# Performance work log

Measured on AMD Instinct MI355X. Metric: run time of the kernel, lower is better.

Reference implementation:

```python
import jax, jax.numpy as jnp
import numpy as np
import math

D_MODEL = 1024
N_HEADS = 16
D_HEAD = D_MODEL // N_HEADS
B, S = 4, 2048


def setup_inputs() -> dict:
    key = jax.random.key(0)
    ks = jax.random.split(key, 9)
    std = 1.0 / math.sqrt(D_MODEL)
    x = jax.random.normal(ks[0], (B, S, D_MODEL), dtype=jnp.float32)
    # causal mask: True = masked out
    mask = jnp.triu(jnp.ones((S, S), dtype=bool), k=1)
    Wq = jax.random.normal(ks[1], (D_MODEL, D_MODEL), jnp.float32) * std
    bq = jnp.zeros((D_MODEL,), jnp.float32)
    Wk = jax.random.normal(ks[2], (D_MODEL, D_MODEL), jnp.float32) * std
    bk = jnp.zeros((D_MODEL,), jnp.float32)
    Wv = jax.random.normal(ks[3], (D_MODEL, D_MODEL), jnp.float32) * std
    bv = jnp.zeros((D_MODEL,), jnp.float32)
    Wo = jax.random.normal(ks[4], (D_MODEL, D_MODEL), jnp.float32) * std
    bo = jnp.zeros((D_MODEL,), jnp.float32)
    return {"x": x, "mask": mask, "Wq": Wq, "bq": bq, "Wk": Wk, "bk": bk,
            "Wv": Wv, "bv": bv, "Wo": Wo, "bo": bo}


def reference(x, mask, Wq, bq, Wk, bk, Wv, bv, Wo, bo):
    b, s, _ = x.shape
    scale = math.sqrt(D_HEAD)
    # projections (Linear: x @ W.T + b), reshape to [b, h, s, d]
    def proj(W, bias):
        y = jnp.einsum('bsd,ed->bse', x, W) + bias
        return y.reshape(b, s, N_HEADS, D_HEAD).transpose(0, 2, 1, 3)
    q = proj(Wq, bq)
    k = proj(Wk, bk)
    v = proj(Wv, bv)
    scores = jnp.einsum('bhqd,bhkd->bhqk', q, k) / scale  # [b,h,s,s]
    scores = jnp.where(mask[None, None, :, :], -jnp.inf, scores)
    attn = jax.nn.softmax(scores, axis=-1)
    # dropout is identity in eval mode
    out = jnp.einsum('bhqk,bhkd->bhqd', attn, v)
    out = out.transpose(0, 2, 1, 3).reshape(b, s, D_MODEL)
    return jnp.einsum('bsd,ed->bse', out, Wo) + bo
```

## Files before the change

### kernel.cpp

```cpp
#include <hip/hip_runtime.h>
#include <stdint.h>

#define NH 16
#define DH 64
#define DM 1024
#define Bz 4
#define Sz 2048
#define NKT 16

typedef __bf16 bf16x8 __attribute__((ext_vector_type(8)));
typedef float f32x4 __attribute__((ext_vector_type(4)));
typedef float f32x16 __attribute__((ext_vector_type(16)));

#define GLD_LDS16(gsrc, ldst)                                             \
    __builtin_amdgcn_global_load_lds(                                     \
        (const __attribute__((address_space(1))) void*)(gsrc),            \
        (__attribute__((address_space(3))) void*)(ldst), 16, 0, 0)

__device__ __forceinline__ unsigned short f2bf(float f) {
    unsigned u = __float_as_uint(f);
    u += 0x7FFFu + ((u >> 16) & 1u);
    return (unsigned short)(u >> 16);
}
__device__ __forceinline__ float bf2f(unsigned short h) {
    return __uint_as_float(((unsigned)h) << 16);
}
__device__ __forceinline__ unsigned pack2bf(float a, float b) {
    return (unsigned)f2bf(a) | ((unsigned)f2bf(b) << 16);
}

__global__ void detect_dtype(const unsigned short* __restrict__ xs,
                             int* __restrict__ flagp)
{
    const int t = threadIdx.x;
    int cnt = 0;
    for (int i = 0; i < 64; i++) {
        const unsigned short h = xs[(t * 64 + i) * 2];
        const int e = (h >> 7) & 0xFF;
        if (h != 0 && e >= 100 && e <= 130) cnt++;
    }
#pragma unroll
    for (int off = 32; off >= 1; off >>= 1)
        cnt += __shfl_xor(cnt, off);
    if (t == 0) *flagp = (cnt < 2048) ? 1 : 0;
}

__global__ __launch_bounds__(256) void convert_inputs(
    const void* s0, const void* s1, const void* s2, const void* s3,
    const void* s4, const void* s5, const void* s6, const void* s7,
    const void* s8,
    unsigned short* d0, unsigned short* d1, unsigned short* d2,
    unsigned short* d3, unsigned short* d4, unsigned short* d5,
    unsigned short* d6, unsigned short* d7, unsigned short* d8,
    const int* __restrict__ flagp)
{
    const void* s; unsigned short* d; int n;
    switch (blockIdx.y) {
        case 0: s = s0; d = d0; n = Bz * Sz * DM; break;
        case 1: s = s1; d = d1; n = DM * DM; break;
        case 2: s = s2; d = d2; n = DM * DM; break;
        case 3: s = s3; d = d3; n = DM * DM; break;
        case 4: s = s4; d = d4; n = DM * DM; break;
        case 5: s = s5; d = d5; n = DM; break;
        case 6: s = s6; d = d6; n = DM; break;
        case 7: s = s7; d = d7; n = DM; break;
        default: s = s8; d = d8; n = DM; break;
    }
    const int flag   = *flagp;
    const int stride = gridDim.x * blockDim.x * 8;
    const int base   = (blockIdx.x * blockDim.x + threadIdx.x) * 8;
    if (flag) {
        const float* sf = (const float*)s;
        for (int i = base; i < n; i += stride) {
            const float4 v0 = *reinterpret_cast<const float4*>(&sf[i]);
            const float4 v1 = *reinterpret_cast<const float4*>(&sf[i + 4]);
            uint4 o;
            o.x = pack2bf(v0.x, v0.y);
            o.y = pack2bf(v0.z, v0.w);
            o.z = pack2bf(v1.x, v1.y);
            o.w = pack2bf(v1.z, v1.w);
            *reinterpret_cast<uint4*>(&d[i]) = o;
        }
    } else {
        const unsigned short* sh = (const unsigned short*)s;
        for (int i = base; i < n; i += stride)
            *reinterpret_cast<uint4*>(&d[i]) = *reinterpret_cast<const uint4*>(&sh[i]);
    }
}


__global__ __launch_bounds__(256, 2) void gemm_qkv(
    const unsigned short* __restrict__ X,
    const unsigned short* __restrict__ Wq,
    const unsigned short* __restrict__ Wk,
    const unsigned short* __restrict__ Wv,
    const unsigned short* __restrict__ bq,
    const unsigned short* __restrict__ bk,
    const unsigned short* __restrict__ bv,
    unsigned short* __restrict__ Qb,
    unsigned short* __restrict__ Kb,
    unsigned short* __restrict__ Vtb)
{
    __shared__ __align__(16) unsigned short As[2][128 * 64];
    __shared__ __align__(16) unsigned short Bs[2][128 * 64];

    const int tid  = threadIdx.x;
    const int w    = tid >> 6, lane = tid & 63;
    const int l31  = lane & 31, half = lane >> 5;
    const int wm   = (w & 1) * 64, wn = (w >> 1) * 64;

    const int flat = (int)(blockIdx.y * gridDim.x + blockIdx.x);
    const int k8   = flat & 7;
    const int m    = flat >> 3;
    const int proj = m >> 6;
    const int mm   = m & 63;
    const int bm   = (k8 * 8 + (mm >> 3)) * 128;
    const int bn   = (mm & 7) * 128;

    const unsigned short* W      = proj == 0 ? Wq : (proj == 1 ? Wk : Wv);
    const unsigned short* bias_p = proj == 0 ? bq : (proj == 1 ? bk : bv);
    const unsigned short* Abase  = X + (size_t)bm * DM;
    const unsigned short* Bbase  = W + (size_t)bn * DM;

    const int sr8 = lane >> 3;
    const int sce = ((lane & 7) ^ sr8) * 8;

    f32x16 acc[2][2];
#pragma unroll
    for (int i = 0; i < 2; i++)
#pragma unroll
        for (int j = 0; j < 2; j++)
#pragma unroll
            for (int e = 0; e < 16; e++)
                acc[i][j][e] = 0.f;

    auto stage = [&](int buf, int kt) {
        const int kc = kt * 64;
#pragma unroll
        for (int t = 0; t < 4; t++) {
            const int r = w * 32 + t * 8;
            GLD_LDS16(&Abase[(size_t)(r + sr8) * DM + kc + sce], &As[buf][r * 64]);
            GLD_LDS16(&Bbase[(size_t)(r + sr8) * DM + kc + sce], &Bs[buf][r * 64]);
        }
    };

    auto frg = [&](const unsigned short* base, int row, int cb) {
        const int cs = cb ^ ((row & 7) << 4);
        return *reinterpret_cast<const bf16x8*>(
            reinterpret_cast<const char*>(base) + row * 128 + cs);
    };

    stage(0, 0);
    asm volatile("s_waitcnt vmcnt(0)" ::: "memory");
    __builtin_amdgcn_s_barrier();
    asm volatile("" ::: "memory");

    for (int T = 0; T < NKT; ++T) {
        if (T < NKT - 1) stage((T + 1) & 1, T + 1);
        const unsigned short* A = &As[T & 1][0];
        const unsigned short* B = &Bs[T & 1][0];
#pragma unroll
        for (int s = 0; s < 4; s++) {
            const int cb = s * 32 + half * 16;
            const bf16x8 a0 = frg(A, wm + l31,      cb);
            const bf16x8 a1 = frg(A, wm + 32 + l31, cb);
            const bf16x8 b0 = frg(B, wn + l31,      cb);
            const bf16x8 b1 = frg(B, wn + 32 + l31, cb);
            acc[0][0] = __builtin_amdgcn_mfma_f32_32x32x16_bf16(a0, b0, acc[0][0], 0, 0, 0);
            acc[0][1] = __builtin_amdgcn_mfma_f32_32x32x16_bf16(a0, b1, acc[0][1], 0, 0, 0);
            acc[1][0] = __builtin_amdgcn_mfma_f32_32x32x16_bf16(a1, b0, acc[1][0], 0, 0, 0);
            acc[1][1] = __builtin_amdgcn_mfma_f32_32x32x16_bf16(a1, b1, acc[1][1], 0, 0, 0);
        }
        asm volatile("s_waitcnt vmcnt(0)" ::: "memory");
        __builtin_amdgcn_s_barrier();
        asm volatile("" ::: "memory");
    }

    if (proj < 2) {
        unsigned short* dst = (proj == 0) ? Qb : Kb;
#pragma unroll
        for (int nj = 0; nj < 2; nj++) {
            const int   e    = bn + wn + nj * 32 + l31;
            const int   h    = e >> 6, dd = e & 63;
            const float bias = bf2f(bias_p[e]);
#pragma unroll
            for (int mi = 0; mi < 2; mi++) {
#pragma unroll
                for (int reg = 0; reg < 16; reg++) {
                    const int mrow = bm + wm + mi * 32 + (reg & 3) + 8 * (reg >> 2) + 4 * half;
                    const int b = mrow >> 11, s = mrow & 2047;
                    dst[((size_t)(b * NH + h) * Sz + s) * DH + dd] = f2bf(acc[mi][nj][reg] + bias);
                }
            }
        }
    } else {
#pragma unroll
        for (int nj = 0; nj < 2; nj++) {
            const int   e    = bn + wn + nj * 32 + l31;
            const int   h    = e >> 6, dd = e & 63;
            const float bias = bf2f(bias_p[e]);
#pragma unroll
            for (int mi = 0; mi < 2; mi++) {
#pragma unroll
                for (int g = 0; g < 4; g++) {
                    const int m0 = bm + wm + mi * 32 + 8 * g + 4 * half;
                    const int b  = m0 >> 11, s0 = m0 & 2047;
                    const unsigned u0 = __float_as_uint(acc[mi][nj][4 * g + 0] + bias) + 0x8000u;
                    const unsigned u1 = __float_as_uint(acc[mi][nj][4 * g + 1] + bias) + 0x8000u;
                    const unsigned u2 = __float_as_uint(acc[mi][nj][4 * g + 2] + bias) + 0x8000u;
                    const unsigned u3 = __float_as_uint(acc[mi][nj][4 * g + 3] + bias) + 0x8000u;
                    uint2 pk;
                    pk.x = __builtin_amdgcn_perm(u1, u0, 0x07060302u);
                    pk.y = __builtin_amdgcn_perm(u3, u2, 0x07060302u);
                    *reinterpret_cast<uint2*>(
                        &Vtb[((size_t)(b * NH + h) * DH + dd) * Sz + s0]) = pk;
                }
            }
        }
    }
}

__global__ __launch_bounds__(512) void flash_attn(
    const unsigned short* __restrict__ Qb,
    const unsigned short* __restrict__ Kb,
    const unsigned short* __restrict__ Vtb,
    unsigned short* __restrict__ AOb)
{
    __shared__ __align__(16) unsigned short Ks[128 * 72];
    __shared__ __align__(16) unsigned short Vs[64 * 136];
    __shared__ __align__(16) unsigned short Ps[128 * 72];

    const int tid  = threadIdx.x;
    const int w    = tid >> 6, lane = tid & 63;
    const int quad = lane >> 4, l15 = lane & 15;

    const int flat = (int)(blockIdx.y * gridDim.x + blockIdx.x);
    const int k8   = flat & 7;
    const int m    = flat >> 3;
    const int bh   = k8 + 8 * (m >> 3);
    const int cA   = m & 7;

    const int srow = tid >> 3;
    const int scc  = (tid & 7) * 8;
    const int hh = bh & 15, bb = bh >> 4;

    for (int pass = 0; pass < 2; pass++) {
        const int chunk = pass ? (15 - cA) : cA;
        const int qb = chunk * 128;
        const int qw = qb + w * 16;

        const size_t qbase = ((size_t)bh * Sz + qw + l15) * DH;
        const bf16x8 qf0 = *reinterpret_cast<const bf16x8*>(&Qb[qbase + quad * 8]);
        const bf16x8 qf1 = *reinterpret_cast<const bf16x8*>(&Qb[qbase + 32 + quad * 8]);

        f32x4 o[4];
#pragma unroll
        for (int jd = 0; jd < 4; jd++) o[jd] = f32x4{0.f, 0.f, 0.f, 0.f};
        float lsum = 0.f;

        const int n_kv = qb + 128;

        auto compute = [&](int kbe) {
            const int  off       = kbe & 127;
            const bool need_mask = (kbe + 64 > qw);
#pragma unroll
            for (int j = 0; j < 4; j++) {
                const bf16x8 kf0 = *reinterpret_cast<const bf16x8*>(&Ks[(off + j * 16 + l15) * 72 + quad * 8]);
                const bf16x8 kf1 = *reinterpret_cast<const bf16x8*>(&Ks[(off + j * 16 + l15) * 72 + 32 + quad * 8]);
                f32x4 st = f32x4{0.f, 0.f, 0.f, 0.f};
                st = __builtin_amdgcn_mfma_f32_16x16x32_bf16(kf0, qf0, st, 0, 0, 0);
                st = __builtin_amdgcn_mfma_f32_16x16x32_bf16(kf1, qf1, st, 0, 0, 0);
                const int qa = qw + l15;
                float p[4];
#pragma unroll
                for (int r = 0; r < 4; r++) {
                    float e = __builtin_amdgcn_exp2f(st[r] * 0.18033688011f);
                    if (need_mask) {
                        const int kv = kbe + j * 16 + quad * 4 + r;
                        e = (kv <= qa) ? e : 0.f;
                    }
                    p[r] = e;
                }
                lsum += (p[0] + p[1]) + (p[2] + p[3]);
                const unsigned u0 = __float_as_uint(p[0]) + 0x8000u;
                const unsigned u1 = __float_as_uint(p[1]) + 0x8000u;
                const unsigned u2 = __float_as_uint(p[2]) + 0x8000u;
                const unsigned u3 = __float_as_uint(p[3]) + 0x8000u;
                const unsigned pk0 = __builtin_amdgcn_perm(u1, u0, 0x07060302u);
                const unsigned pk1 = __builtin_amdgcn_perm(u3, u2, 0x07060302u);
                const int prow = (w * 16 + l15) * 72 + j * 16 + quad * 4;
                *reinterpret_cast<unsigned*>(&Ps[prow])     = pk0;
                *reinterpret_cast<unsigned*>(&Ps[prow + 2]) = pk1;
            }

            asm volatile("s_waitcnt lgkmcnt(0)" ::: "memory");

            const bf16x8 pf0 = *reinterpret_cast<const bf16x8*>(&Ps[(w * 16 + l15) * 72 + quad * 8]);
            const bf16x8 pf1 = *reinterpret_cast<const bf16x8*>(&Ps[(w * 16 + l15) * 72 + 32 + quad * 8]);
#pragma unroll
            for (int jd = 0; jd < 4; jd++) {
                const bf16x8 vf0 = *reinterpret_cast<const bf16x8*>(&Vs[(jd * 16 + l15) * 136 + off + quad * 8]);
                const bf16x8 vf1 = *reinterpret_cast<const bf16x8*>(&Vs[(jd * 16 + l15) * 136 + off + 32 + quad * 8]);
                o[jd] = __builtin_amdgcn_mfma_f32_16x16x32_bf16(pf0, vf0, o[jd], 0, 0, 0);
                o[jd] = __builtin_amdgcn_mfma_f32_16x16x32_bf16(pf1, vf1, o[jd], 0, 0, 0);
            }
        };

        uint4 kr0 = *reinterpret_cast<const uint4*>(&Kb[((size_t)bh * Sz + srow) * DH + scc]);
        uint4 kr1 = *reinterpret_cast<const uint4*>(&Kb[((size_t)bh * Sz + 64 + srow) * DH + scc]);
        uint4 vr0 = *reinterpret_cast<const uint4*>(&Vtb[((size_t)bh * DH + srow) * Sz + scc]);
        uint4 vr1 = *reinterpret_cast<const uint4*>(&Vtb[((size_t)bh * DH + srow) * Sz + 64 + scc]);

        for (int kb = 0; kb < n_kv; kb += 128) {
            __syncthreads();
            *reinterpret_cast<uint4*>(&Ks[srow * 72 + scc])        = kr0;
            *reinterpret_cast<uint4*>(&Ks[(64 + srow) * 72 + scc]) = kr1;
            *reinterpret_cast<uint4*>(&Vs[srow * 136 + scc])       = vr0;
            *reinterpret_cast<uint4*>(&Vs[srow * 136 + 64 + scc])  = vr1;
            if (kb + 128 < n_kv) {
                kr0 = *reinterpret_cast<const uint4*>(&Kb[((size_t)bh * Sz + kb + 128 + srow) * DH + scc]);
                kr1 = *reinterpret_cast<const uint4*>(&Kb[((size_t)bh * Sz + kb + 192 + srow) * DH + scc]);
                vr0 = *reinterpret_cast<const uint4*>(&Vtb[((size_t)bh * DH + srow) * Sz + kb + 128 + scc]);
                vr1 = *reinterpret_cast<const uint4*>(&Vtb[((size_t)bh * DH + srow) * Sz + kb + 192 + scc]);
            }
            asm volatile("s_waitcnt lgkmcnt(0)" ::: "memory");
            __builtin_amdgcn_s_barrier();
            asm volatile("" ::: "memory");
            if (kb <= qw + 15)      compute(kb);
            if (kb + 64 <= qw + 15) compute(kb + 64);
        }

        lsum += __shfl_xor(lsum, 16);
        lsum += __shfl_xor(lsum, 32);

        float linv[4];
#pragma unroll
        for (int r = 0; r < 4; r++)
            linv[r] = 1.0f / __shfl(lsum, quad * 4 + r);
#pragma unroll
        for (int jd = 0; jd < 4; jd++) {
#pragma unroll
            for (int r = 0; r < 4; r++) {
                const int s = qw + quad * 4 + r;
                AOb[((size_t)(bb * Sz + s)) * DM + hh * DH + jd * 16 + l15] =
                    f2bf(o[jd][r] * linv[r]);
            }
        }
    }
}

__global__ __launch_bounds__(256, 4) void gemm_out(
    const unsigned short* __restrict__ Ain,
    const unsigned short* __restrict__ W,
    const unsigned short* __restrict__ bo,
    void* __restrict__ outv,
    const int* __restrict__ flagp)
{
    __shared__ __align__(16) unsigned short As[128 * 64];
    __shared__ __align__(16) unsigned short Bs[128 * 64];

    const int tid  = threadIdx.x;
    const int w    = tid >> 6, lane = tid & 63;
    const int l31  = lane & 31, half = lane >> 5;
    const int wm   = (w & 1) * 64, wn = (w >> 1) * 64;

    const int flat = (int)(blockIdx.y * gridDim.x + blockIdx.x);
    const int k8   = flat & 7;
    const int m    = flat >> 3;
    const int bm   = (k8 * 8 + (m >> 3)) * 128;
    const int bn   = (m & 7) * 128;

    const unsigned short* Abase = Ain + (size_t)bm * DM;
    const unsigned short* Bbase = W   + (size_t)bn * DM;

    const int sr8 = lane >> 3;
    const int sce = ((lane & 7) ^ sr8) * 8;

    f32x16 acc[2][2];
#pragma unroll
    for (int i = 0; i < 2; i++)
#pragma unroll
        for (int j = 0; j < 2; j++)
#pragma unroll
            for (int e = 0; e < 16; e++)
                acc[i][j][e] = 0.f;

    auto stage = [&](int kt) {
        const int kc = kt * 64;
#pragma unroll
        for (int t = 0; t < 4; t++) {
            const int r = w * 32 + t * 8;
            GLD_LDS16(&Abase[(size_t)(r + sr8) * DM + kc + sce], &As[r * 64]);
            GLD_LDS16(&Bbase[(size_t)(r + sr8) * DM + kc + sce], &Bs[r * 64]);
        }
    };

    auto frg = [&](const unsigned short* base, int row, int cb) {
        const int cs = cb ^ ((row & 7) << 4);
        return *reinterpret_cast<const bf16x8*>(
            reinterpret_cast<const char*>(base) + row * 128 + cs);
    };

    for (int T = 0; T < NKT; ++T) {
        stage(T);
        asm volatile("s_waitcnt vmcnt(0)" ::: "memory");
        __builtin_amdgcn_s_barrier();
        asm volatile("" ::: "memory");
#pragma unroll
        for (int s = 0; s < 4; s++) {
            const int cb = s * 32 + half * 16;
            const bf16x8 a0 = frg(As, wm + l31,      cb);
            const bf16x8 a1 = frg(As, wm + 32 + l31, cb);
            const bf16x8 b0 = frg(Bs, wn + l31,      cb);
            const bf16x8 b1 = frg(Bs, wn + 32 + l31, cb);
            acc[0][0] = __builtin_amdgcn_mfma_f32_32x32x16_bf16(a0, b0, acc[0][0], 0, 0, 0);
            acc[0][1] = __builtin_amdgcn_mfma_f32_32x32x16_bf16(a0, b1, acc[0][1], 0, 0, 0);
            acc[1][0] = __builtin_amdgcn_mfma_f32_32x32x16_bf16(a1, b0, acc[1][0], 0, 0, 0);
            acc[1][1] = __builtin_amdgcn_mfma_f32_32x32x16_bf16(a1, b1, acc[1][1], 0, 0, 0);
        }
        __builtin_amdgcn_s_barrier();
        asm volatile("" ::: "memory");
    }

    const int flag = *flagp;
    float*          outf = (float*)outv;
    unsigned short* outh = (unsigned short*)outv;
#pragma unroll
    for (int nj = 0; nj < 2; nj++) {
        const int   e    = bn + wn + nj * 32 + l31;
        const float bias = bf2f(bo[e]);
#pragma unroll
        for (int mi = 0; mi < 2; mi++) {
#pragma unroll
            for (int reg = 0; reg < 16; reg++) {
                const int   mrow = bm + wm + mi * 32 + (reg & 3) + 8 * (reg >> 2) + 4 * half;
                const float v = acc[mi][nj][reg] + bias;
                if (flag) outf[(size_t)mrow * DM + e] = v;
                else      outh[(size_t)mrow * DM + e] = f2bf(v);
            }
        }
    }
}

extern "C" void kernel_launch(void* const* d_in, const int* in_sizes, int n_in,
                              void* d_out, int out_size, void* d_ws, size_t ws_size,
                              hipStream_t stream) {
    const void* x = nullptr;
    const void* Wsrc[4] = {nullptr, nullptr, nullptr, nullptr};
    const void* bsrc[4] = {nullptr, nullptr, nullptr, nullptr};
    int nw = 0, nb = 0;
    for (int i = 0; i < n_in; i++) {
        const int sz = in_sizes[i];
        if (sz == Bz * Sz * DM)            { if (!x) x = d_in[i]; }
        else if (sz == DM * DM)            { if (nw < 4) Wsrc[nw++] = d_in[i]; }
        else if (sz == DM)                 { if (nb < 4) bsrc[nb++] = d_in[i]; }
    }

    char* wsb = (char*)d_ws;
    int*  flagp = (int*)wsb;
    unsigned short* Xc  = (unsigned short*)(wsb + 16);
    const size_t NX = (size_t)Bz * Sz * DM;
    const size_t NW = (size_t)DM * DM;
    unsigned short* Wc0 = Xc  + NX;
    unsigned short* Wc1 = Wc0 + NW;
    unsigned short* Wc2 = Wc1 + NW;
    unsigned short* Wc3 = Wc2 + NW;
    unsigned short* bc0 = Wc3 + NW;
    unsigned short* bc1 = bc0 + DM;
    unsigned short* bc2 = bc1 + DM;
    unsigned short* bc3 = bc2 + DM;
    unsigned short* Qb  = bc3 + DM;
    const size_t SZ = (size_t)Bz * NH * Sz * DH;
    unsigned short* Kb  = Qb  + SZ;
    unsigned short* Vtb = Kb  + SZ;
    unsigned short* AOb = Vtb + SZ;

    detect_dtype<<<1, 64, 0, stream>>>((const unsigned short*)x, flagp);
    convert_inputs<<<dim3(512, 9), 256, 0, stream>>>(
        x, Wsrc[0], Wsrc[1], Wsrc[2], Wsrc[3],
        bsrc[0], bsrc[1], bsrc[2], bsrc[3],
        Xc, Wc0, Wc1, Wc2, Wc3, bc0, bc1, bc2, bc3, flagp);

    gemm_qkv <<<dim3(24, 64), 256, 0, stream>>>(Xc, Wc0, Wc1, Wc2, bc0, bc1, bc2, Qb, Kb, Vtb);
    flash_attn<<<dim3(8, 64), 512, 0, stream>>>(Qb, Kb, Vtb, AOb);
    gemm_out <<<dim3(8, 64), 256, 0, stream>>>(AOb, Wc3, bc3, d_out, flagp);
}
```

Measured before the change: 279.4 us.

## Switch flash attention to 32x32x16 MFMA with register-resident P

Rewrites the attention kernel so each of 4 waves handles 32 query rows using 32x32x16 bf16 MFMA instructions instead of 8 waves of 16-row 16x16x32 tiles. The probability tile now stays in registers and is rearranged with a cross-half lane shuffle into the B-operand layout, which removes the Ps LDS buffer and its write/read round trip. The block shrinks to 256 threads with a 3-blocks-per-SM bound, and K/V staging uses wider per-thread loads. This trades more registers per wave and the shuffle overhead for fewer MFMA issues and less LDS traffic.

```diff
diff --git a/kernel.cpp b/kernel.cpp
--- a/kernel.cpp
+++ b/kernel.cpp
@@ -88,7 +88,6 @@
     }
 }
 
-
 __global__ __launch_bounds__(256, 2) void gemm_qkv(
     const unsigned short* __restrict__ X,
     const unsigned short* __restrict__ Wq,
@@ -220,7 +219,7 @@
     }
 }
 
-__global__ __launch_bounds__(512) void flash_attn(
+__global__ __launch_bounds__(256, 3) void flash_attn(
     const unsigned short* __restrict__ Qb,
     const unsigned short* __restrict__ Kb,
     const unsigned short* __restrict__ Vtb,
@@ -228,11 +227,10 @@
 {
     __shared__ __align__(16) unsigned short Ks[128 * 72];
     __shared__ __align__(16) unsigned short Vs[64 * 136];
-    __shared__ __align__(16) unsigned short Ps[128 * 72];
 
     const int tid  = threadIdx.x;
     const int w    = tid >> 6, lane = tid & 63;
-    const int quad = lane >> 4, l15 = lane & 15;
+    const int l31  = lane & 31, half = lane >> 5;
 
     const int flat = (int)(blockIdx.y * gridDim.x + blockIdx.x);
     const int k8   = flat & 7;
@@ -240,22 +238,24 @@
     const int bh   = k8 + 8 * (m >> 3);
     const int cA   = m & 7;
 
-    const int srow = tid >> 3;
-    const int scc  = (tid & 7) * 8;
+    const int srK = tid >> 1, scK = (tid & 1) * 32;
+    const int srV = tid >> 2, scV = (tid & 3) * 32;
     const int hh = bh & 15, bb = bh >> 4;
 
     for (int pass = 0; pass < 2; pass++) {
         const int chunk = pass ? (15 - cA) : cA;
         const int qb = chunk * 128;
-        const int qw = qb + w * 16;
-
-        const size_t qbase = ((size_t)bh * Sz + qw + l15) * DH;
-        const bf16x8 qf0 = *reinterpret_cast<const bf16x8*>(&Qb[qbase + quad * 8]);
-        const bf16x8 qf1 = *reinterpret_cast<const bf16x8*>(&Qb[qbase + 32 + quad * 8]);
-
-        f32x4 o[4];
-#pragma unroll
-        for (int jd = 0; jd < 4; jd++) o[jd] = f32x4{0.f, 0.f, 0.f, 0.f};
+        const int qw = qb + w * 32;
+
+        const size_t qrow = ((size_t)bh * Sz + qw + l31) * DH;
+        bf16x8 qf0 = *reinterpret_cast<const bf16x8*>(&Qb[qrow +  0 + 8 * half]);
+        bf16x8 qf1 = *reinterpret_cast<const bf16x8*>(&Qb[qrow + 16 + 8 * half]);
+        bf16x8 qf2 = *reinterpret_cast<const bf16x8*>(&Qb[qrow + 32 + 8 * half]);
+        bf16x8 qf3 = *reinterpret_cast<const bf16x8*>(&Qb[qrow + 48 + 8 * half]);
+
+        f32x16 o0, o1;
+#pragma unroll
+        for (int e = 0; e < 16; e++) { o0[e] = 0.f; o1[e] = 0.f; }
         float lsum = 0.f;
 
         const int n_kv = qb + 128;
@@ -263,88 +263,110 @@
         auto compute = [&](int kbe) {
             const int  off       = kbe & 127;
             const bool need_mask = (kbe + 64 > qw);
-#pragma unroll
-            for (int j = 0; j < 4; j++) {
-                const bf16x8 kf0 = *reinterpret_cast<const bf16x8*>(&Ks[(off + j * 16 + l15) * 72 + quad * 8]);
-                const bf16x8 kf1 = *reinterpret_cast<const bf16x8*>(&Ks[(off + j * 16 + l15) * 72 + 32 + quad * 8]);
-                f32x4 st = f32x4{0.f, 0.f, 0.f, 0.f};
-                st = __builtin_amdgcn_mfma_f32_16x16x32_bf16(kf0, qf0, st, 0, 0, 0);
-                st = __builtin_amdgcn_mfma_f32_16x16x32_bf16(kf1, qf1, st, 0, 0, 0);
-                const int qa = qw + l15;
-                float p[4];
-#pragma unroll
-                for (int r = 0; r < 4; r++) {
-                    float e = __builtin_amdgcn_exp2f(st[r] * 0.18033688011f);
+            const int  qa        = qw + l31;
+#pragma unroll
+            for (int s2 = 0; s2 < 2; s2++) {
+                f32x16 st;
+#pragma unroll
+                for (int e = 0; e < 16; e++) st[e] = 0.f;
+#pragma unroll
+                for (int t = 0; t < 4; t++) {
+                    const bf16x8 kf = *reinterpret_cast<const bf16x8*>(
+                        &Ks[(off + 32 * s2 + l31) * 72 + 16 * t + 8 * half]);
+                    if (t == 0) st = __builtin_amdgcn_mfma_f32_32x32x16_bf16(kf, qf0, st, 0, 0, 0);
+                    if (t == 1) st = __builtin_amdgcn_mfma_f32_32x32x16_bf16(kf, qf1, st, 0, 0, 0);
+                    if (t == 2) st = __builtin_amdgcn_mfma_f32_32x32x16_bf16(kf, qf2, st, 0, 0, 0);
+                    if (t == 3) st = __builtin_amdgcn_mfma_f32_32x32x16_bf16(kf, qf3, st, 0, 0, 0);
+                }
+                const int kvb = kbe + 32 * s2 + 4 * half;
+                unsigned D[8], E[8];
+#pragma unroll
+                for (int r2 = 0; r2 < 8; r2++) {
+                    const int r = 2 * r2;
+                    float p0 = __builtin_amdgcn_exp2f(st[r]     * 0.18033688011f);
+                    float p1 = __builtin_amdgcn_exp2f(st[r + 1] * 0.18033688011f);
                     if (need_mask) {
-                        const int kv = kbe + j * 16 + quad * 4 + r;
-                        e = (kv <= qa) ? e : 0.f;
+                        const int kv0 = kvb + (r & 3) + 8 * (r >> 2);
+                        p0 = (kv0     <= qa) ? p0 : 0.f;
+                        p1 = (kv0 + 1 <= qa) ? p1 : 0.f;
                     }
-                    p[r] = e;
+                    lsum += p0 + p1;
+                    const unsigned u0 = __float_as_uint(p0) + 0x8000u;
+                    const unsigned u1 = __float_as_uint(p1) + 0x8000u;
+                    D[r2] = __builtin_amdgcn_perm(u1, u0, 0x07060302u);
                 }
-                lsum += (p[0] + p[1]) + (p[2] + p[3]);
-                const unsigned u0 = __float_as_uint(p[0]) + 0x8000u;
-                const unsigned u1 = __float_as_uint(p[1]) + 0x8000u;
-                const unsigned u2 = __float_as_uint(p[2]) + 0x8000u;
-                const unsigned u3 = __float_as_uint(p[3]) + 0x8000u;
-                const unsigned pk0 = __builtin_amdgcn_perm(u1, u0, 0x07060302u);
-                const unsigned pk1 = __builtin_amdgcn_perm(u3, u2, 0x07060302u);
-                const int prow = (w * 16 + l15) * 72 + j * 16 + quad * 4;
-                *reinterpret_cast<unsigned*>(&Ps[prow])     = pk0;
-                *reinterpret_cast<unsigned*>(&Ps[prow + 2]) = pk1;
-            }
-
-            asm volatile("s_waitcnt lgkmcnt(0)" ::: "memory");
-
-            const bf16x8 pf0 = *reinterpret_cast<const bf16x8*>(&Ps[(w * 16 + l15) * 72 + quad * 8]);
-            const bf16x8 pf1 = *reinterpret_cast<const bf16x8*>(&Ps[(w * 16 + l15) * 72 + 32 + quad * 8]);
-#pragma unroll
-            for (int jd = 0; jd < 4; jd++) {
-                const bf16x8 vf0 = *reinterpret_cast<const bf16x8*>(&Vs[(jd * 16 + l15) * 136 + off + quad * 8]);
-                const bf16x8 vf1 = *reinterpret_cast<const bf16x8*>(&Vs[(jd * 16 + l15) * 136 + off + 32 + quad * 8]);
-                o[jd] = __builtin_amdgcn_mfma_f32_16x16x32_bf16(pf0, vf0, o[jd], 0, 0, 0);
-                o[jd] = __builtin_amdgcn_mfma_f32_16x16x32_bf16(pf1, vf1, o[jd], 0, 0, 0);
+#pragma unroll
+                for (int r2 = 0; r2 < 8; r2++)
+                    E[r2] = (unsigned)__shfl_xor((int)D[r2], 32);
+
+#pragma unroll
+                for (int t2 = 0; t2 < 2; t2++) {
+                    uint4 pw;
+                    pw.x = half ? E[4 * t2 + 2] : D[4 * t2 + 0];
+                    pw.y = half ? E[4 * t2 + 3] : D[4 * t2 + 1];
+                    pw.z = half ? D[4 * t2 + 2] : E[4 * t2 + 0];
+                    pw.w = half ? D[4 * t2 + 3] : E[4 * t2 + 1];
+                    bf16x8 pf;
+                    __builtin_memcpy(&pf, &pw, 16);
+                    const int kvc = off + 32 * s2 + 16 * t2;
+                    const bf16x8 vf0 = *reinterpret_cast<const bf16x8*>(
+                        &Vs[(l31) * 136 + kvc + 8 * half]);
+                    const bf16x8 vf1 = *reinterpret_cast<const bf16x8*>(
+                        &Vs[(32 + l31) * 136 + kvc + 8 * half]);
+                    o0 = __builtin_amdgcn_mfma_f32_32x32x16_bf16(pf, vf0, o0, 0, 0, 0);
+                    o1 = __builtin_amdgcn_mfma_f32_32x32x16_bf16(pf, vf1, o1, 0, 0, 0);
+                }
             }
         };
 
-        uint4 kr0 = *reinterpret_cast<const uint4*>(&Kb[((size_t)bh * Sz + srow) * DH + scc]);
-        uint4 kr1 = *reinterpret_cast<const uint4*>(&Kb[((size_t)bh * Sz + 64 + srow) * DH + scc]);
-        uint4 vr0 = *reinterpret_cast<const uint4*>(&Vtb[((size_t)bh * DH + srow) * Sz + scc]);
-        uint4 vr1 = *reinterpret_cast<const uint4*>(&Vtb[((size_t)bh * DH + srow) * Sz + 64 + scc]);
+        uint4 kr0 = *reinterpret_cast<const uint4*>(&Kb[((size_t)bh * Sz + srK) * DH + scK]);
+        uint4 kr1 = *reinterpret_cast<const uint4*>(&Kb[((size_t)bh * Sz + srK) * DH + scK + 8]);
+        uint4 kr2 = *reinterpret_cast<const uint4*>(&Kb[((size_t)bh * Sz + srK) * DH + scK + 16]);
+        uint4 kr3 = *reinterpret_cast<const uint4*>(&Kb[((size_t)bh * Sz + srK) * DH + scK + 24]);
+        uint4 vr0 = *reinterpret_cast<const uint4*>(&Vtb[((size_t)bh * DH + srV) * Sz + scV]);
+        uint4 vr1 = *reinterpret_cast<const uint4*>(&Vtb[((size_t)bh * DH + srV) * Sz + scV + 8]);
+        uint4 vr2 = *reinterpret_cast<const uint4*>(&Vtb[((size_t)bh * DH + srV) * Sz + scV + 16]);
+        uint4 vr3 = *reinterpret_cast<const uint4*>(&Vtb[((size_t)bh * DH + srV) * Sz + scV + 24]);
 
         for (int kb = 0; kb < n_kv; kb += 128) {
             __syncthreads();
-            *reinterpret_cast<uint4*>(&Ks[srow * 72 + scc])        = kr0;
-            *reinterpret_cast<uint4*>(&Ks[(64 + srow) * 72 + scc]) = kr1;
-            *reinterpret_cast<uint4*>(&Vs[srow * 136 + scc])       = vr0;
-            *reinterpret_cast<uint4*>(&Vs[srow * 136 + 64 + scc])  = vr1;
+            *reinterpret_cast<uint4*>(&Ks[srK * 72 + scK])      = kr0;
+            *reinterpret_cast<uint4*>(&Ks[srK * 72 + scK + 8])  = kr1;
+            *reinterpret_cast<uint4*>(&Ks[srK * 72 + scK + 16]) = kr2;
+            *reinterpret_cast<uint4*>(&Ks[srK * 72 + scK + 24]) = kr3;
+            *reinterpret_cast<uint4*>(&Vs[srV * 136 + scV])      = vr0;
+            *reinterpret_cast<uint4*>(&Vs[srV * 136 + scV + 8])  = vr1;
+            *reinterpret_cast<uint4*>(&Vs[srV * 136 + scV + 16]) = vr2;
+            *reinterpret_cast<uint4*>(&Vs[srV * 136 + scV + 24]) = vr3;
             if (kb + 128 < n_kv) {
-                kr0 = *reinterpret_cast<const uint4*>(&Kb[((size_t)bh * Sz + kb + 128 + srow) * DH + scc]);
-                kr1 = *reinterpret_cast<const uint4*>(&Kb[((size_t)bh * Sz + kb + 192 + srow) * DH + scc]);
-                vr0 = *reinterpret_cast<const uint4*>(&Vtb[((size_t)bh * DH + srow) * Sz + kb + 128 + scc]);
-                vr1 = *reinterpret_cast<const uint4*>(&Vtb[((size_t)bh * DH + srow) * Sz + kb + 192 + scc]);
+                const size_t kg = (size_t)bh * Sz + kb + 128 + srK;
+                const size_t vg = (size_t)bh * DH + srV;
+                kr0 = *reinterpret_cast<const uint4*>(&Kb[kg * DH + scK]);
+                kr1 = *reinterpret_cast<const uint4*>(&Kb[kg * DH + scK + 8]);
+                kr2 = *reinterpret_cast<const uint4*>(&Kb[kg * DH + scK + 16]);
+                kr3 = *reinterpret_cast<const uint4*>(&Kb[kg * DH + scK + 24]);
+                vr0 = *reinterpret_cast<const uint4*>(&Vtb[vg * Sz + kb + 128 + scV]);
+                vr1 = *reinterpret_cast<const uint4*>(&Vtb[vg * Sz + kb + 128 + scV + 8]);
+                vr2 = *reinterpret_cast<const uint4*>(&Vtb[vg * Sz + kb + 128 + scV + 16]);
+                vr3 = *reinterpret_cast<const uint4*>(&Vtb[vg * Sz + kb + 128 + scV + 24]);
             }
             asm volatile("s_waitcnt lgkmcnt(0)" ::: "memory");
             __builtin_amdgcn_s_barrier();
             asm volatile("" ::: "memory");
-            if (kb <= qw + 15)      compute(kb);
-            if (kb + 64 <= qw + 15) compute(kb + 64);
-        }
-
-        lsum += __shfl_xor(lsum, 16);
+            if (kb <= qw + 31)      compute(kb);
+            if (kb + 64 <= qw + 31) compute(kb + 64);
+        }
+
         lsum += __shfl_xor(lsum, 32);
-
-        float linv[4];
-#pragma unroll
-        for (int r = 0; r < 4; r++)
-            linv[r] = 1.0f / __shfl(lsum, quad * 4 + r);
-#pragma unroll
-        for (int jd = 0; jd < 4; jd++) {
-#pragma unroll
-            for (int r = 0; r < 4; r++) {
-                const int s = qw + quad * 4 + r;
-                AOb[((size_t)(bb * Sz + s)) * DM + hh * DH + jd * 16 + l15] =
-                    f2bf(o[jd][r] * linv[r]);
-            }
+        const float linv = 1.0f / lsum;
+
+#pragma unroll
+        for (int r = 0; r < 16; r++) {
+            const int   ql = (r & 3) + 8 * (r >> 2) + 4 * half;
+            const float li = __shfl(linv, ql);
+            const size_t rowb = ((size_t)(bb * Sz + qw + ql)) * DM + hh * DH;
+            AOb[rowb + l31]      = f2bf(o0[r] * li);
+            AOb[rowb + 32 + l31] = f2bf(o1[r] * li);
         }
     }
 }
@@ -482,6 +504,6 @@
         Xc, Wc0, Wc1, Wc2, Wc3, bc0, bc1, bc2, bc3, flagp);
 
     gemm_qkv <<<dim3(24, 64), 256, 0, stream>>>(Xc, Wc0, Wc1, Wc2, bc0, bc1, bc2, Qb, Kb, Vtb);
-    flash_attn<<<dim3(8, 64), 512, 0, stream>>>(Qb, Kb, Vtb, AOb);
+    flash_attn<<<dim3(8, 64), 256, 0, stream>>>(Qb, Kb, Vtb, AOb);
     gemm_out <<<dim3(8, 64), 256, 0, stream>>>(AOb, Wc3, bc3, d_out, flagp);
 }
```

After: 286.0 us. 1.02x slower.
